# Kernel optimization log

Measured on AMD Instinct MI355X. Metric: run time of the kernel, lower is better.

## Reference

```python
import jax, jax.numpy as jnp
import numpy as np

NUM_HEADS = 2
D = 512
D_HID = 2048


def _layer_norm(x, g, b, eps):
    mu = jnp.mean(x, axis=-1, keepdims=True)
    var = jnp.var(x, axis=-1, keepdims=True)
    return (x - mu) * jax.lax.rsqrt(var + eps) * g + b


def _attn_block(Q, K, V, resnet, Wq, Wk, Wv, ln_g, ln_b, w1, w2, fln_g, fln_b):
    # Linear projections (torch Linear: x @ W.T), no bias
    q = Q @ Wq.T
    k = K @ Wk.T
    v = V @ Wv.T
    B, N, C = q.shape
    gs = C // NUM_HEADS  # group size per head
    # split channels into heads == reshape [B,N,H,gs] -> [B,H,N,gs]
    qh = q.reshape(B, N, NUM_HEADS, gs).transpose(0, 2, 1, 3)
    kh = k.reshape(B, K.shape[1], NUM_HEADS, gs).transpose(0, 2, 1, 3)
    vh = v.reshape(B, V.shape[1], NUM_HEADS, gs).transpose(0, 2, 1, 3)
    scores = jnp.einsum('bhqd,bhkd->bhqk', qh, kh) / jnp.sqrt(jnp.asarray(gs, q.dtype))
    attn = jax.nn.softmax(scores, axis=-1)
    out = jnp.einsum('bhqk,bhkd->bhqd', attn, vh)
    # concat heads back to channel dim
    out = out.transpose(0, 2, 1, 3).reshape(B, N, C)
    x = out + resnet
    x = _layer_norm(x, ln_g, ln_b, 1e-5)
    # FFN (dropout is identity in eval mode)
    residual = x
    y = jax.nn.relu(x @ w1.T) @ w2.T
    y = y + residual
    y = _layer_norm(y, fln_g, fln_b, 1e-6)
    return y


def setup_inputs() -> dict:
    key = jax.random.key(0)
    ks = jax.random.split(key, 16)
    B, N = 4, 2048
    Fm = jax.random.normal(ks[0], (B, N, D), dtype=jnp.float32)
    Fs = jax.random.normal(ks[1], (B, N, D), dtype=jnp.float32)
    Fq = jax.random.normal(ks[2], (B, N, D), dtype=jnp.float32)
    s = 0.02
    Wq = jax.random.normal(ks[3], (3, D, D), dtype=jnp.float32) * s
    Wk = jax.random.normal(ks[4], (3, D, D), dtype=jnp.float32) * s
    Wv = jax.random.normal(ks[5], (3, D, D), dtype=jnp.float32) * s
    ln_g = jnp.ones((3, D), dtype=jnp.float32)
    ln_b = jnp.zeros((3, D), dtype=jnp.float32)
    w1 = jax.random.normal(ks[6], (3, D_HID, D), dtype=jnp.float32) * s
    w2 = jax.random.normal(ks[7], (3, D, D_HID), dtype=jnp.float32) * s
    fln_g = jnp.ones((3, D), dtype=jnp.float32)
    fln_b = jnp.zeros((3, D), dtype=jnp.float32)
    return {"Fm": Fm, "Fs": Fs, "Fq": Fq, "Wq": Wq, "Wk": Wk, "Wv": Wv,
            "ln_g": ln_g, "ln_b": ln_b, "w1": w1, "w2": w2,
            "fln_g": fln_g, "fln_b": fln_b, "out_dim": 512}


def reference(Fm, Fs, Fq, Wq, Wk, Wv, ln_g, ln_b, w1, w2, fln_g, fln_b, out_dim):
    def blk(i, Q, K, V, resnet):
        return _attn_block(Q, K, V, resnet, Wq[i], Wk[i], Wv[i], ln_g[i], ln_b[i],
                           w1[i], w2[i], fln_g[i], fln_b[i])
    css = blk(0, Fs, Fs, Fm, Fm)
    cqq = blk(1, Fq, Fq, Fq, Fq)
    csq = blk(2, cqq, Fs, css, css)
    return csq
```

## Files before the change

kernel.cpp:

```cpp
#include <hip/hip_runtime.h>

typedef __bf16 bf16_t;
typedef __bf16 bf16x8 __attribute__((ext_vector_type(8)));
typedef float  f32x4  __attribute__((ext_vector_type(4)));

#define GAS __attribute__((address_space(1)))
#define LAS __attribute__((address_space(3)))

enum { EPI_BF16 = 0, EPI_RELU = 1 };

__global__ void probe_dtype(const unsigned* __restrict__ lng_bits, int* __restrict__ flag)
{
    *flag = (lng_bits[0] == 0x3F800000u) ? 0 : 1;
}

__global__ __launch_bounds__(256) void conv_any3(
    const void* __restrict__ s0, const void* __restrict__ s1, const void* __restrict__ s2,
    bf16_t* __restrict__ d0, bf16_t* __restrict__ d1, bf16_t* __restrict__ d2,
    const int* __restrict__ flag, int n8)
{
    int i = blockIdx.x * 256 + threadIdx.x;
    if (i >= n8) return;
    const void* src = (blockIdx.z == 0) ? s0 : (blockIdx.z == 1) ? s1 : s2;
    bf16_t*    dst = (blockIdx.z == 0) ? d0 : (blockIdx.z == 1) ? d1 : d2;
    if (*flag == 0) {
        const float4* s = (const float4*)src;
        float4 a = s[i * 2], b = s[i * 2 + 1];
        bf16x8 o = { (bf16_t)a.x, (bf16_t)a.y, (bf16_t)a.z, (bf16_t)a.w,
                     (bf16_t)b.x, (bf16_t)b.y, (bf16_t)b.z, (bf16_t)b.w };
        ((bf16x8*)dst)[i] = o;
    } else {
        ((uint4*)dst)[i] = ((const uint4*)src)[i];
    }
}

__global__ __launch_bounds__(256) void widen_ln4(
    const void* __restrict__ a, const void* __restrict__ b,
    const void* __restrict__ c, const void* __restrict__ d,
    float* __restrict__ dst, const int* __restrict__ flag, int n)
{
    int i = blockIdx.x * 256 + threadIdx.x;
    int seg = i / n, j = i - seg * n;
    if (seg >= 4) return;
    const void* s = (seg == 0) ? a : (seg == 1) ? b : (seg == 2) ? c : d;
    dst[i] = (*flag == 0) ? ((const float*)s)[j]
                          : (float)((const bf16_t*)s)[j];
}

template<int EPI, int TMv, int TNv, bool MULTI>
__global__ __launch_bounds__(256) void gemm_bt(
    const bf16_t* __restrict__ A0, const bf16_t* __restrict__ A1, const bf16_t* __restrict__ A2,
    const bf16_t* __restrict__ B0, const bf16_t* __restrict__ B1, const bf16_t* __restrict__ B2,
    bf16_t* __restrict__ C0, bf16_t* __restrict__ C1, bf16_t* __restrict__ C2,
    int K, int lda, int ldb, int ldc,
    long sAb, long sAh, long sBb, long sBh, long sCb, long sCh,
    float scale)
{
    constexpr int MF = TMv / 32, NF = TNv / 32;
    constexpr int STG = 2 * (TMv + TNv) * 32;
    constexpr int RPK = TMv * TNv;
    constexpr int SME = (STG > RPK) ? STG : RPK;
    __shared__ __align__(16) bf16_t smem[SME];
    bf16_t* Asb = smem;
    bf16_t* Bsb = smem + 2 * TMv * 32;

    const bf16_t* A; const bf16_t* B; bf16_t* C; long cOff = 0;
    if constexpr (MULTI) {
        const int z = blockIdx.z;
        A = (z == 0) ? A0 : (z == 1) ? A1 : A2;
        B = (z == 0) ? B0 : (z == 1) ? B1 : B2;
        C = (z == 0) ? C0 : (z == 1) ? C1 : C2;
    } else {
        const long zb = blockIdx.z >> 1, zh = blockIdx.z & 1;
        A = A0 + zb * sAb + zh * sAh;
        B = B0 + zb * sBb + zh * sBh;
        C = C0; cOff = zb * sCb + zh * sCh;
    }

    int m_t, n_t;
    {
        const int gx = gridDim.x, gy = gridDim.y;
        if ((gy & 7) == 0) {
            const int L = blockIdx.y * gx + blockIdx.x;
            const int band_h = gy >> 3;
            const int r = L >> 3;
            m_t = (L & 7) * band_h + (r % band_h);
            n_t = r / band_h;
        } else { m_t = blockIdx.y; n_t = blockIdx.x; }
    }
    const int n0 = n_t * TNv;
    const int m0 = m_t * TMv;

    const int tid  = threadIdx.x;
    const int wave = tid >> 6, lane = tid & 63;
    const int wm = (wave >> 1) * (TMv / 2);
    const int wn = (wave & 1) * (TNv / 2);
    const int lrow = lane & 15, lquad = lane >> 4;
    const int rq   = (lquad ^ ((lrow >> 1) & 3)) * 8;
    const int drow = lane >> 2;
    const int dcol = (((lane & 3) ^ ((lane >> 3) & 3))) * 8;

    f32x4 acc[MF][NF];
    #pragma unroll
    for (int i = 0; i < MF; i++)
        #pragma unroll
        for (int j = 0; j < NF; j++) acc[i][j] = (f32x4){0.f, 0.f, 0.f, 0.f};

    const bf16_t* aP = A + (long)(m0 + wave * (TMv / 4) + drow) * lda + dcol;
    const bf16_t* bP = B + (long)(n0 + wave * (TNv / 4) + drow) * ldb + dcol;
    bf16_t* asW = Asb + wave * (TMv / 4) * 32;
    bf16_t* bsW = Bsb + wave * (TNv / 4) * 32;

    for (int kk = 0; kk < K; kk += 64) {
        __syncthreads();
        #pragma unroll
        for (int p = 0; p < 2; p++) {
            #pragma unroll
            for (int i = 0; i < TMv / 64; i++)
                __builtin_amdgcn_global_load_lds(
                    (GAS void*)(aP + p * 32 + (long)i * 16 * lda),
                    (LAS void*)(asW + p * TMv * 32 + i * 16 * 32), 16, 0, 0);
            #pragma unroll
            for (int i = 0; i < TNv / 64; i++)
                __builtin_amdgcn_global_load_lds(
                    (GAS void*)(bP + p * 32 + (long)i * 16 * ldb),
                    (LAS void*)(bsW + p * TNv * 32 + i * 16 * 32), 16, 0, 0);
        }
        aP += 64; bP += 64;
        __syncthreads();

        #pragma unroll
        for (int p = 0; p < 2; p++) {
            bf16x8 af[MF], bfr[NF];
            #pragma unroll
            for (int mi = 0; mi < MF; mi++)
                af[mi] = *(const bf16x8*)&Asb[(p * TMv + wm + mi * 16 + lrow) * 32 + rq];
            #pragma unroll
            for (int ni = 0; ni < NF; ni++)
                bfr[ni] = *(const bf16x8*)&Bsb[(p * TNv + wn + ni * 16 + lrow) * 32 + rq];
            #pragma unroll
            for (int mi = 0; mi < MF; mi++)
                #pragma unroll
                for (int ni = 0; ni < NF; ni++)
                    acc[mi][ni] = __builtin_amdgcn_mfma_f32_16x16x32_bf16(
                        af[mi], bfr[ni], acc[mi][ni], 0, 0, 0);
        }
    }

    __syncthreads();
    #pragma unroll
    for (int mi = 0; mi < MF; mi++)
        #pragma unroll
        for (int ni = 0; ni < NF; ni++)
            #pragma unroll
            for (int r = 0; r < 4; r++) {
                float v = acc[mi][ni][r] * scale;
                if (EPI == EPI_RELU) v = fmaxf(v, 0.f);
                smem[(wm + mi * 16 + lquad * 4 + r) * TNv + wn + ni * 16 + lrow] = (bf16_t)v;
            }
    __syncthreads();
    constexpr int TPR = TNv / 8;
    constexpr int RPP = 256 / TPR;
    const int srow = tid / TPR;
    const int scol = (tid % TPR) * 8;
    #pragma unroll
    for (int pass = 0; pass < TMv / RPP; pass++) {
        const int rr = pass * RPP + srow;
        bf16x8 vv = *(const bf16x8*)&smem[rr * TNv + scol];
        *(bf16x8*)&C[cOff + (long)(m0 + rr) * ldc + n0 + scol] = vv;
    }
}

__global__ __launch_bounds__(256) void transpose_v(
    const bf16_t* __restrict__ v, bf16_t* __restrict__ vT)
{
    __shared__ bf16_t t[64][72];
    const int m0 = blockIdx.x * 64;
    const int c0 = blockIdx.y * 64;
    const int tid = threadIdx.x;
    const int rr = tid >> 3;
    const int cc = (tid & 7) * 8;
    #pragma unroll
    for (int i = 0; i < 2; i++) {
        int r = rr + i * 32;
        *(uint4*)&t[r][cc] = *(const uint4*)&v[(long)(m0 + r) * 512 + c0 + cc];
    }
    __syncthreads();
    const int b = m0 >> 11;
    #pragma unroll
    for (int i = 0; i < 2; i++) {
        int d  = rr + i * 32;
        int gc = c0 + d;
        int h  = gc >> 8, dd = gc & 255;
        int n  = (m0 & 2047) + cc;
        bf16x8 tmp;
        #pragma unroll
        for (int j = 0; j < 8; j++) tmp[j] = t[cc + j][d];
        *(bf16x8*)&vT[((long)(b * 2 + h) * 256 + dd) * 2048 + n] = tmp;
    }
}

__global__ __launch_bounds__(256) void softmax_rows(bf16_t* __restrict__ buf)
{
    const long base = (long)blockIdx.x * 2048;
    const int tid = threadIdx.x;
    const int wave = tid >> 6, lane = tid & 63;
    __shared__ float red[8];
    bf16x8 x = *(const bf16x8*)&buf[base + tid * 8];
    float v[8];
    float mx = -1e30f;
    #pragma unroll
    for (int j = 0; j < 8; j++) { v[j] = (float)x[j]; mx = fmaxf(mx, v[j]); }
    for (int off = 32; off; off >>= 1) mx = fmaxf(mx, __shfl_xor(mx, off));
    if (lane == 0) red[wave] = mx;
    __syncthreads();
    mx = fmaxf(fmaxf(red[0], red[1]), fmaxf(red[2], red[3]));
    float s = 0.f;
    #pragma unroll
    for (int j = 0; j < 8; j++) { v[j] = __expf(v[j] - mx); s += v[j]; }
    for (int off = 32; off; off >>= 1) s += __shfl_xor(s, off);
    if (lane == 0) red[4 + wave] = s;
    __syncthreads();
    s = red[4] + red[5] + red[6] + red[7];
    const float inv = 1.f / s;
    bf16x8 y;
    #pragma unroll
    for (int j = 0; j < 8; j++) y[j] = (bf16_t)(v[j] * inv);
    *(bf16x8*)&buf[base + tid * 8] = y;
}

template<typename OutT>
__global__ __launch_bounds__(256) void add_ln(
    const bf16_t* xin, const bf16_t* __restrict__ res,
    const float* __restrict__ g, const float* __restrict__ bias,
    OutT* out, float eps)
{
    const int wave = threadIdx.x >> 6, lane = threadIdx.x & 63;
    const long row = (long)blockIdx.x * 4 + wave;
    const long base = row * 512 + lane * 8;
    bf16x8 a8 = *(const bf16x8*)&xin[base];
    bf16x8 r8 = *(const bf16x8*)&res[base];
    float v[8];
    #pragma unroll
    for (int j = 0; j < 8; j++) v[j] = (float)a8[j] + (float)r8[j];
    float s = 0.f, s2 = 0.f;
    #pragma unroll
    for (int j = 0; j < 8; j++) { s += v[j]; s2 += v[j] * v[j]; }
    for (int off = 32; off; off >>= 1) { s += __shfl_xor(s, off); s2 += __shfl_xor(s2, off); }
    const float mu  = s * (1.f / 512.f);
    const float var = s2 * (1.f / 512.f) - mu * mu;
    const float rs  = rsqrtf(var + eps);
    const int c0 = lane * 8;
    float4 g0 = *(const float4*)&g[c0];
    float4 g1 = *(const float4*)&g[c0 + 4];
    float4 b0 = *(const float4*)&bias[c0];
    float4 b1 = *(const float4*)&bias[c0 + 4];
    float gv[8] = { g0.x, g0.y, g0.z, g0.w, g1.x, g1.y, g1.z, g1.w };
    float bv[8] = { b0.x, b0.y, b0.z, b0.w, b1.x, b1.y, b1.z, b1.w };
    #pragma unroll
    for (int j = 0; j < 8; j++)
        out[base + j] = (OutT)((v[j] - mu) * rs * gv[j] + bv[j]);
}

extern "C" void kernel_launch(void* const* d_in, const int* in_sizes, int n_in,
                              void* d_out, int out_size, void* d_ws, size_t ws_size,
                              hipStream_t stream)
{
    const void* Fm    = d_in[0];
    const void* Fs    = d_in[1];
    const void* Fq    = d_in[2];
    const void* Wq    = d_in[3];
    const void* Wk    = d_in[4];
    const void* Wv    = d_in[5];
    const void* ln_g  = d_in[6];
    const void* ln_b  = d_in[7];
    const void* w1    = d_in[8];
    const void* w2    = d_in[9];
    const void* fln_g = d_in[10];
    const void* fln_b = d_in[11];
    (void)in_sizes; (void)n_in; (void)out_size; (void)ws_size;

    char* ws = (char*)d_ws;
    size_t off = 0;
    auto take = [&](size_t bytes) {
        char* p = ws + off;
        off += (bytes + 255) & ~(size_t)255;
        return p;
    };
    const size_t NT = 8192ul * 512;

    int*    flag = (int*)take(256);
    float*  lnw  = (float*)take(4ul * 1536 * 4);
    bf16_t* Fm_b = (bf16_t*)take(NT * 2);
    bf16_t* Fs_b = (bf16_t*)take(NT * 2);
    bf16_t* Fq_b = (bf16_t*)take(NT * 2);
    bf16_t* wqb  = (bf16_t*)take(3ul * 512 * 512 * 2);
    bf16_t* wkb  = (bf16_t*)take(3ul * 512 * 512 * 2);
    bf16_t* wvb  = (bf16_t*)take(3ul * 512 * 512 * 2);
    bf16_t* w1b  = (bf16_t*)take(3ul * 2048 * 512 * 2);
    bf16_t* w2b  = (bf16_t*)take(3ul * 512 * 2048 * 2);
    bf16_t* q_b  = (bf16_t*)take(NT * 2);
    bf16_t* k_b  = (bf16_t*)take(NT * 2);
    char*   R_v  = take(NT * 2);
    char*   R_vt = take(NT * 2);
    char*   R_sc = take(8ul * 2048 * 2048 * 2);

    bf16_t* css = Fm_b;
    bf16_t* cqq = Fq_b;

    bf16_t* v_b = (bf16_t*)R_v;
    bf16_t* ao  = (bf16_t*)R_v;
    bf16_t* x_b = (bf16_t*)R_v;
    bf16_t* vT  = (bf16_t*)R_vt;
    bf16_t* y_b = (bf16_t*)R_vt;
    bf16_t* sc  = (bf16_t*)R_sc;
    bf16_t* h_b = (bf16_t*)R_sc;

    dim3 blk(256);
    probe_dtype<<<dim3(1), dim3(1), 0, stream>>>((const unsigned*)ln_g, flag);

    conv_any3<<<dim3(2048, 1, 3), blk, 0, stream>>>(
        Fm, Fs, Fq, Fm_b, Fs_b, Fq_b, flag, (int)(NT / 8));
    conv_any3<<<dim3(384, 1, 3), blk, 0, stream>>>(
        Wq, Wk, Wv, wqb, wkb, wvb, flag, (int)(3ul * 512 * 512 / 8));
    conv_any3<<<dim3(1536, 1, 2), blk, 0, stream>>>(
        w1, w2, w2, w1b, w2b, w2b, flag, (int)(3ul * 2048 * 512 / 8));
    widen_ln4<<<dim3(24), blk, 0, stream>>>(ln_g, ln_b, fln_g, fln_b, lnw, flag, 1536);

    auto block = [&](const bf16_t* Q, const bf16_t* Kin, const bf16_t* V,
                     const bf16_t* res, int i, void* outp, bool out_f32) {
        const bf16_t* wqr = wqb + (size_t)i * 512 * 512;
        const bf16_t* wkr = wkb + (size_t)i * 512 * 512;
        const bf16_t* wvr = wvb + (size_t)i * 512 * 512;
        const bf16_t* w1r = w1b + (size_t)i * 2048 * 512;
        const bf16_t* w2r = w2b + (size_t)i * 512 * 2048;
        const float* g1 = lnw + i * 512;
        const float* b1 = lnw + 1536 + i * 512;
        const float* g2 = lnw + 2 * 1536 + i * 512;
        const float* b2 = lnw + 3 * 1536 + i * 512;

        gemm_bt<EPI_BF16, 128, 64, true><<<dim3(8, 64, 3), blk, 0, stream>>>(
            Q, Kin, V, wqr, wkr, wvr, q_b, k_b, v_b,
            512, 512, 512, 512, 0, 0, 0, 0, 0, 0, 1.f);
        transpose_v<<<dim3(128, 8, 1), blk, 0, stream>>>(v_b, vT);

        gemm_bt<EPI_BF16, 128, 128, false><<<dim3(16, 16, 8), blk, 0, stream>>>(
            q_b, nullptr, nullptr, k_b, nullptr, nullptr, sc, nullptr, nullptr,
            256, 512, 512, 2048,
            1048576L, 256L, 1048576L, 256L, 8388608L, 4194304L, 0.0625f);
        softmax_rows<<<dim3(16384), blk, 0, stream>>>(sc);
        gemm_bt<EPI_BF16, 128, 64, false><<<dim3(4, 16, 8), blk, 0, stream>>>(
            sc, nullptr, nullptr, vT, nullptr, nullptr, ao, nullptr, nullptr,
            2048, 2048, 2048, 512,
            8388608L, 4194304L, 1048576L, 524288L, 1048576L, 256L, 1.f);
        add_ln<bf16_t><<<dim3(2048), blk, 0, stream>>>(ao, res, g1, b1, x_b, 1e-5f);

        gemm_bt<EPI_RELU, 128, 128, false><<<dim3(16, 64, 1), blk, 0, stream>>>(
            x_b, nullptr, nullptr, w1r, nullptr, nullptr, h_b, nullptr, nullptr,
            512, 512, 512, 2048, 0, 0, 0, 0, 0, 0, 1.f);
        gemm_bt<EPI_BF16, 128, 64, false><<<dim3(8, 64, 1), blk, 0, stream>>>(
            h_b, nullptr, nullptr, w2r, nullptr, nullptr, y_b, nullptr, nullptr,
            2048, 2048, 2048, 512, 0, 0, 0, 0, 0, 0, 1.f);
        if (out_f32)
            add_ln<float><<<dim3(2048), blk, 0, stream>>>(
                y_b, x_b, g2, b2, (float*)outp, 1e-6f);
        else
            add_ln<bf16_t><<<dim3(2048), blk, 0, stream>>>(
                y_b, x_b, g2, b2, (bf16_t*)outp, 1e-6f);
    };

    block(Fs_b, Fs_b, Fm_b, Fm_b, 0, css, false);
    block(Fq_b, Fq_b, Fq_b, Fq_b, 1, cqq, false);
    block(cqq,  Fs_b, css,  css,  2, d_out, true);
}
```

Before: 697.8 us.

## Batch independent attention blocks 0 and 1 together and fuse V transpose into projection

```diff
diff --git a/kernel.cpp b/kernel.cpp
--- a/kernel.cpp
+++ b/kernel.cpp
@@ -2,12 +2,19 @@
 
 typedef __bf16 bf16_t;
 typedef __bf16 bf16x8 __attribute__((ext_vector_type(8)));
+typedef __bf16 bf16x4 __attribute__((ext_vector_type(4)));
 typedef float  f32x4  __attribute__((ext_vector_type(4)));
 
 #define GAS __attribute__((address_space(1)))
 #define LAS __attribute__((address_space(3)))
 
 enum { EPI_BF16 = 0, EPI_RELU = 1 };
+
+struct GPtrs {
+    const bf16_t* A[6];
+    const bf16_t* B[6];
+    bf16_t*       C[6];
+};
 
 __global__ void probe_dtype(const unsigned* __restrict__ lng_bits, int* __restrict__ flag)
 {
@@ -47,12 +54,9 @@
                           : (float)((const bf16_t*)s)[j];
 }
 
-template<int EPI, int TMv, int TNv, bool MULTI>
+template<int EPI, int TMv, int TNv, bool TABLE, int ZH, bool VT>
 __global__ __launch_bounds__(256) void gemm_bt(
-    const bf16_t* __restrict__ A0, const bf16_t* __restrict__ A1, const bf16_t* __restrict__ A2,
-    const bf16_t* __restrict__ B0, const bf16_t* __restrict__ B1, const bf16_t* __restrict__ B2,
-    bf16_t* __restrict__ C0, bf16_t* __restrict__ C1, bf16_t* __restrict__ C2,
-    int K, int lda, int ldb, int ldc,
+    GPtrs P, int K, int lda, int ldb, int ldc,
     long sAb, long sAh, long sBb, long sBh, long sCb, long sCh,
     float scale)
 {
@@ -64,17 +68,16 @@
     bf16_t* Asb = smem;
     bf16_t* Bsb = smem + 2 * TMv * 32;
 
+    const int z = blockIdx.z;
     const bf16_t* A; const bf16_t* B; bf16_t* C; long cOff = 0;
-    if constexpr (MULTI) {
-        const int z = blockIdx.z;
-        A = (z == 0) ? A0 : (z == 1) ? A1 : A2;
-        B = (z == 0) ? B0 : (z == 1) ? B1 : B2;
-        C = (z == 0) ? C0 : (z == 1) ? C1 : C2;
+    if constexpr (TABLE) {
+        A = P.A[z]; B = P.B[z]; C = P.C[z];
     } else {
-        const long zb = blockIdx.z >> 1, zh = blockIdx.z & 1;
-        A = A0 + zb * sAb + zh * sAh;
-        B = B0 + zb * sBb + zh * sBh;
-        C = C0; cOff = zb * sCb + zh * sCh;
+        const int half = z / ZH, zz = z % ZH;
+        const long zb = zz >> 1, zh = zz & 1;
+        A = P.A[half] + zb * sAb + zh * sAh;
+        B = P.B[half] + zb * sBb + zh * sBh;
+        C = P.C[half]; cOff = zb * sCb + zh * sCh;
     }
 
     int m_t, n_t;
@@ -145,6 +148,24 @@
                     acc[mi][ni] = __builtin_amdgcn_mfma_f32_16x16x32_bf16(
                         af[mi], bfr[ni], acc[mi][ni], 0, 0, 0);
         }
+    }
+
+    if (VT && (z % 3 == 2)) {
+        #pragma unroll
+        for (int mi = 0; mi < MF; mi++)
+            #pragma unroll
+            for (int ni = 0; ni < NF; ni++) {
+                const int mr = m0 + wm + mi * 16 + lquad * 4;
+                const int nc = n0 + wn + ni * 16 + lrow;
+                const int b = mr >> 11, s = mr & 2047;
+                const int h = nc >> 8,  d = nc & 255;
+                bf16x4 t = { (bf16_t)(acc[mi][ni][0]),
+                             (bf16_t)(acc[mi][ni][1]),
+                             (bf16_t)(acc[mi][ni][2]),
+                             (bf16_t)(acc[mi][ni][3]) };
+                *(bf16x4*)&C[(((long)(b * 2 + h) * 256 + d) << 11) + s] = t;
+            }
+        return;
     }
 
     __syncthreads();
@@ -171,35 +192,6 @@
     }
 }
 
-__global__ __launch_bounds__(256) void transpose_v(
-    const bf16_t* __restrict__ v, bf16_t* __restrict__ vT)
-{
-    __shared__ bf16_t t[64][72];
-    const int m0 = blockIdx.x * 64;
-    const int c0 = blockIdx.y * 64;
-    const int tid = threadIdx.x;
-    const int rr = tid >> 3;
-    const int cc = (tid & 7) * 8;
-    #pragma unroll
-    for (int i = 0; i < 2; i++) {
-        int r = rr + i * 32;
-        *(uint4*)&t[r][cc] = *(const uint4*)&v[(long)(m0 + r) * 512 + c0 + cc];
-    }
-    __syncthreads();
-    const int b = m0 >> 11;
-    #pragma unroll
-    for (int i = 0; i < 2; i++) {
-        int d  = rr + i * 32;
-        int gc = c0 + d;
-        int h  = gc >> 8, dd = gc & 255;
-        int n  = (m0 & 2047) + cc;
-        bf16x8 tmp;
-        #pragma unroll
-        for (int j = 0; j < 8; j++) tmp[j] = t[cc + j][d];
-        *(bf16x8*)&vT[((long)(b * 2 + h) * 256 + dd) * 2048 + n] = tmp;
-    }
-}
-
 __global__ __launch_bounds__(256) void softmax_rows(bf16_t* __restrict__ buf)
 {
     const long base = (long)blockIdx.x * 2048;
@@ -229,14 +221,20 @@
     *(bf16x8*)&buf[base + tid * 8] = y;
 }
 
-template<typename OutT>
-__global__ __launch_bounds__(256) void add_ln(
-    const bf16_t* xin, const bf16_t* __restrict__ res,
-    const float* __restrict__ g, const float* __restrict__ bias,
-    OutT* out, float eps)
+__global__ __launch_bounds__(256) void add_ln2(
+    const bf16_t* xA, const bf16_t* rA, const float* gA, const float* bA, bf16_t* oA,
+    const bf16_t* xB, const bf16_t* rB, const float* gB, const float* bB, bf16_t* oB,
+    float eps, int splitRows)
 {
     const int wave = threadIdx.x >> 6, lane = threadIdx.x & 63;
-    const long row = (long)blockIdx.x * 4 + wave;
+    long row = (long)blockIdx.x * 4 + wave;
+    const bf16_t* xin; const bf16_t* res; const float* g; const float* bias; bf16_t* out;
+    if (row >= splitRows) {
+        row -= splitRows;
+        xin = xB; res = rB; g = gB; bias = bB; out = oB;
+    } else {
+        xin = xA; res = rA; g = gA; bias = bA; out = oA;
+    }
     const long base = row * 512 + lane * 8;
     bf16x8 a8 = *(const bf16x8*)&xin[base];
     bf16x8 r8 = *(const bf16x8*)&res[base];
@@ -259,7 +257,39 @@
     float bv[8] = { b0.x, b0.y, b0.z, b0.w, b1.x, b1.y, b1.z, b1.w };
     #pragma unroll
     for (int j = 0; j < 8; j++)
-        out[base + j] = (OutT)((v[j] - mu) * rs * gv[j] + bv[j]);
+        out[base + j] = (bf16_t)((v[j] - mu) * rs * gv[j] + bv[j]);
+}
+
+__global__ __launch_bounds__(256) void add_ln_f32(
+    const bf16_t* xin, const bf16_t* __restrict__ res,
+    const float* __restrict__ g, const float* __restrict__ bias,
+    float* out, float eps)
+{
+    const int wave = threadIdx.x >> 6, lane = threadIdx.x & 63;
+    const long row = (long)blockIdx.x * 4 + wave;
+    const long base = row * 512 + lane * 8;
+    bf16x8 a8 = *(const bf16x8*)&xin[base];
+    bf16x8 r8 = *(const bf16x8*)&res[base];
+    float v[8];
+    #pragma unroll
+    for (int j = 0; j < 8; j++) v[j] = (float)a8[j] + (float)r8[j];
+    float s = 0.f, s2 = 0.f;
+    #pragma unroll
+    for (int j = 0; j < 8; j++) { s += v[j]; s2 += v[j] * v[j]; }
+    for (int off = 32; off; off >>= 1) { s += __shfl_xor(s, off); s2 += __shfl_xor(s2, off); }
+    const float mu  = s * (1.f / 512.f);
+    const float var = s2 * (1.f / 512.f) - mu * mu;
+    const float rs  = rsqrtf(var + eps);
+    const int c0 = lane * 8;
+    float4 g0 = *(const float4*)&g[c0];
+    float4 g1 = *(const float4*)&g[c0 + 4];
+    float4 b0 = *(const float4*)&bias[c0];
+    float4 b1 = *(const float4*)&bias[c0 + 4];
+    float gv[8] = { g0.x, g0.y, g0.z, g0.w, g1.x, g1.y, g1.z, g1.w };
+    float bv[8] = { b0.x, b0.y, b0.z, b0.w, b1.x, b1.y, b1.z, b1.w };
+    #pragma unroll
+    for (int j = 0; j < 8; j++)
+        out[base + j] = (v[j] - mu) * rs * gv[j] + bv[j];
 }
 
 extern "C" void kernel_launch(void* const* d_in, const int* in_sizes, int n_in,
@@ -299,22 +329,25 @@
     bf16_t* wvb  = (bf16_t*)take(3ul * 512 * 512 * 2);
     bf16_t* w1b  = (bf16_t*)take(3ul * 2048 * 512 * 2);
     bf16_t* w2b  = (bf16_t*)take(3ul * 512 * 2048 * 2);
-    bf16_t* q_b  = (bf16_t*)take(NT * 2);
-    bf16_t* k_b  = (bf16_t*)take(NT * 2);
-    char*   R_v  = take(NT * 2);
-    char*   R_vt = take(NT * 2);
-    char*   R_sc = take(8ul * 2048 * 2048 * 2);
-
+    bf16_t* q0   = (bf16_t*)take(NT * 2);
+    bf16_t* k0   = (bf16_t*)take(NT * 2);
+    bf16_t* q1   = (bf16_t*)take(NT * 2);
+    bf16_t* k1   = (bf16_t*)take(NT * 2);
+    bf16_t* vT0  = (bf16_t*)take(NT * 2);
+    bf16_t* vT1  = (bf16_t*)take(NT * 2);
+    bf16_t* scb  = (bf16_t*)take(2ul * 8 * 2048 * 2048 * 2);
+
+    bf16_t* sc0 = scb;
+    bf16_t* sc1 = scb + 8ul * 2048 * 2048;
+    bf16_t* ao0 = q0;  bf16_t* ao1 = q1;
+    bf16_t* x0  = k0;  bf16_t* x1  = k1;
+    bf16_t* h0  = scb; bf16_t* h1  = scb + 16ul * 1024 * 1024;
+    bf16_t* y0  = vT0; bf16_t* y1  = vT1;
     bf16_t* css = Fm_b;
     bf16_t* cqq = Fq_b;
-
-    bf16_t* v_b = (bf16_t*)R_v;
-    bf16_t* ao  = (bf16_t*)R_v;
-    bf16_t* x_b = (bf16_t*)R_v;
-    bf16_t* vT  = (bf16_t*)R_vt;
-    bf16_t* y_b = (bf16_t*)R_vt;
-    bf16_t* sc  = (bf16_t*)R_sc;
-    bf16_t* h_b = (bf16_t*)R_sc;
+    bf16_t* q2  = q0;  bf16_t* k2  = k0;  bf16_t* vT2 = vT0;
+    bf16_t* sc2 = scb; bf16_t* ao2 = q1;  bf16_t* x2  = k1;
+    bf16_t* h2  = scb + 32ul * 1024 * 1024;  bf16_t* y2 = vT1;
 
     dim3 blk(256);
     probe_dtype<<<dim3(1), dim3(1), 0, stream>>>((const unsigned*)ln_g, flag);
@@ -327,49 +360,94 @@
         w1, w2, w2, w1b, w2b, w2b, flag, (int)(3ul * 2048 * 512 / 8));
     widen_ln4<<<dim3(24), blk, 0, stream>>>(ln_g, ln_b, fln_g, fln_b, lnw, flag, 1536);
 
-    auto block = [&](const bf16_t* Q, const bf16_t* Kin, const bf16_t* V,
-                     const bf16_t* res, int i, void* outp, bool out_f32) {
-        const bf16_t* wqr = wqb + (size_t)i * 512 * 512;
-        const bf16_t* wkr = wkb + (size_t)i * 512 * 512;
-        const bf16_t* wvr = wvb + (size_t)i * 512 * 512;
-        const bf16_t* w1r = w1b + (size_t)i * 2048 * 512;
-        const bf16_t* w2r = w2b + (size_t)i * 512 * 2048;
-        const float* g1 = lnw + i * 512;
-        const float* b1 = lnw + 1536 + i * 512;
-        const float* g2 = lnw + 2 * 1536 + i * 512;
-        const float* b2 = lnw + 3 * 1536 + i * 512;
-
-        gemm_bt<EPI_BF16, 128, 64, true><<<dim3(8, 64, 3), blk, 0, stream>>>(
-            Q, Kin, V, wqr, wkr, wvr, q_b, k_b, v_b,
-            512, 512, 512, 512, 0, 0, 0, 0, 0, 0, 1.f);
-        transpose_v<<<dim3(128, 8, 1), blk, 0, stream>>>(v_b, vT);
-
-        gemm_bt<EPI_BF16, 128, 128, false><<<dim3(16, 16, 8), blk, 0, stream>>>(
-            q_b, nullptr, nullptr, k_b, nullptr, nullptr, sc, nullptr, nullptr,
-            256, 512, 512, 2048,
+    auto W  = [&](bf16_t* base, int i, size_t n) { return (const bf16_t*)(base + (size_t)i * n); };
+    const float* g1[3]; const float* b1[3]; const float* g2[3]; const float* b2[3];
+    for (int i = 0; i < 3; i++) {
+        g1[i] = lnw + i * 512;            b1[i] = lnw + 1536 + i * 512;
+        g2[i] = lnw + 2 * 1536 + i * 512; b2[i] = lnw + 3 * 1536 + i * 512;
+    }
+
+    {
+        GPtrs P{};
+        P.A[0] = Fs_b; P.A[1] = Fs_b; P.A[2] = Fm_b;
+        P.A[3] = Fq_b; P.A[4] = Fq_b; P.A[5] = Fq_b;
+        P.B[0] = W(wqb, 0, 512*512); P.B[1] = W(wkb, 0, 512*512); P.B[2] = W(wvb, 0, 512*512);
+        P.B[3] = W(wqb, 1, 512*512); P.B[4] = W(wkb, 1, 512*512); P.B[5] = W(wvb, 1, 512*512);
+        P.C[0] = q0; P.C[1] = k0; P.C[2] = vT0;
+        P.C[3] = q1; P.C[4] = k1; P.C[5] = vT1;
+        gemm_bt<EPI_BF16, 128, 64, true, 1, true><<<dim3(8, 64, 6), blk, 0, stream>>>(
+            P, 512, 512, 512, 512, 0, 0, 0, 0, 0, 0, 1.f);
+    }
+    {
+        GPtrs P{}; P.A[0] = q0; P.A[1] = q1; P.B[0] = k0; P.B[1] = k1;
+        P.C[0] = sc0; P.C[1] = sc1;
+        gemm_bt<EPI_BF16, 128, 128, false, 8, false><<<dim3(16, 16, 16), blk, 0, stream>>>(
+            P, 256, 512, 512, 2048,
             1048576L, 256L, 1048576L, 256L, 8388608L, 4194304L, 0.0625f);
-        softmax_rows<<<dim3(16384), blk, 0, stream>>>(sc);
-        gemm_bt<EPI_BF16, 128, 64, false><<<dim3(4, 16, 8), blk, 0, stream>>>(
-            sc, nullptr, nullptr, vT, nullptr, nullptr, ao, nullptr, nullptr,
-            2048, 2048, 2048, 512,
+    }
+    softmax_rows<<<dim3(32768), blk, 0, stream>>>(scb);
+    {
+        GPtrs P{}; P.A[0] = sc0; P.A[1] = sc1; P.B[0] = vT0; P.B[1] = vT1;
+        P.C[0] = ao0; P.C[1] = ao1;
+        gemm_bt<EPI_BF16, 128, 64, false, 8, false><<<dim3(4, 16, 16), blk, 0, stream>>>(
+            P, 2048, 2048, 2048, 512,
             8388608L, 4194304L, 1048576L, 524288L, 1048576L, 256L, 1.f);
-        add_ln<bf16_t><<<dim3(2048), blk, 0, stream>>>(ao, res, g1, b1, x_b, 1e-5f);
-
-        gemm_bt<EPI_RELU, 128, 128, false><<<dim3(16, 64, 1), blk, 0, stream>>>(
-            x_b, nullptr, nullptr, w1r, nullptr, nullptr, h_b, nullptr, nullptr,
-            512, 512, 512, 2048, 0, 0, 0, 0, 0, 0, 1.f);
-        gemm_bt<EPI_BF16, 128, 64, false><<<dim3(8, 64, 1), blk, 0, stream>>>(
-            h_b, nullptr, nullptr, w2r, nullptr, nullptr, y_b, nullptr, nullptr,
-            2048, 2048, 2048, 512, 0, 0, 0, 0, 0, 0, 1.f);
-        if (out_f32)
-            add_ln<float><<<dim3(2048), blk, 0, stream>>>(
-                y_b, x_b, g2, b2, (float*)outp, 1e-6f);
-        else
-            add_ln<bf16_t><<<dim3(2048), blk, 0, stream>>>(
-                y_b, x_b, g2, b2, (bf16_t*)outp, 1e-6f);
-    };
-
-    block(Fs_b, Fs_b, Fm_b, Fm_b, 0, css, false);
-    block(Fq_b, Fq_b, Fq_b, Fq_b, 1, cqq, false);
-    block(cqq,  Fs_b, css,  css,  2, d_out, true);
-}
+    }
+    add_ln2<<<dim3(4096), blk, 0, stream>>>(
+        ao0, Fm_b, g1[0], b1[0], x0,
+        ao1, Fq_b, g1[1], b1[1], x1, 1e-5f, 8192);
+    {
+        GPtrs P{}; P.A[0] = x0; P.A[1] = x1;
+        P.B[0] = W(w1b, 0, 2048*512); P.B[1] = W(w1b, 1, 2048*512);
+        P.C[0] = h0; P.C[1] = h1;
+        gemm_bt<EPI_RELU, 128, 128, false, 1, false><<<dim3(16, 64, 2), blk, 0, stream>>>(
+            P, 512, 512, 512, 2048, 0, 0, 0, 0, 0, 0, 1.f);
+    }
+    {
+        GPtrs P{}; P.A[0] = h0; P.A[1] = h1;
+        P.B[0] = W(w2b, 0, 512*2048); P.B[1] = W(w2b, 1, 512*2048);
+        P.C[0] = y0; P.C[1] = y1;
+        gemm_bt<EPI_BF16, 128, 64, false, 1, false><<<dim3(8, 64, 2), blk, 0, stream>>>(
+            P, 2048, 2048, 2048, 512, 0, 0, 0, 0, 0, 0, 1.f);
+    }
+    add_ln2<<<dim3(4096), blk, 0, stream>>>(
+        y0, x0, g2[0], b2[0], css,
+        y1, x1, g2[1], b2[1], cqq, 1e-6f, 8192);
+
+    {
+        GPtrs P{};
+        P.A[0] = cqq; P.A[1] = Fs_b; P.A[2] = css;
+        P.B[0] = W(wqb, 2, 512*512); P.B[1] = W(wkb, 2, 512*512); P.B[2] = W(wvb, 2, 512*512);
+        P.C[0] = q2; P.C[1] = k2; P.C[2] = vT2;
+        gemm_bt<EPI_BF16, 128, 64, true, 1, true><<<dim3(8, 64, 3), blk, 0, stream>>>(
+            P, 512, 512, 512, 512, 0, 0, 0, 0, 0, 0, 1.f);
+    }
+    {
+        GPtrs P{}; P.A[0] = q2; P.B[0] = k2; P.C[0] = sc2;
+        gemm_bt<EPI_BF16, 128, 128, false, 8, false><<<dim3(16, 16, 8), blk, 0, stream>>>(
+            P, 256, 512, 512, 2048,
+            1048576L, 256L, 1048576L, 256L, 8388608L, 4194304L, 0.0625f);
+    }
+    softmax_rows<<<dim3(16384), blk, 0, stream>>>(sc2);
+    {
+        GPtrs P{}; P.A[0] = sc2; P.B[0] = vT2; P.C[0] = ao2;
+        gemm_bt<EPI_BF16, 128, 64, false, 8, false><<<dim3(4, 16, 8), blk, 0, stream>>>(
+            P, 2048, 2048, 2048, 512,
+            8388608L, 4194304L, 1048576L, 524288L, 1048576L, 256L, 1.f);
+    }
+    add_ln2<<<dim3(2048), blk, 0, stream>>>(
+        ao2, css, g1[2], b1[2], x2,
+        ao2, css, g1[2], b1[2], x2, 1e-5f, 1 << 30);
+    {
+        GPtrs P{}; P.A[0] = x2; P.B[0] = W(w1b, 2, 2048*512); P.C[0] = h2;
+        gemm_bt<EPI_RELU, 128, 128, false, 1, false><<<dim3(16, 64, 1), blk, 0, stream>>>(
+            P, 512, 512, 512, 2048, 0, 0, 0, 0, 0, 0, 1.f);
+    }
+    {
+        GPtrs P{}; P.A[0] = h2; P.B[0] = W(w2b, 2, 512*2048); P.C[0] = y2;
+        gemm_bt<EPI_BF16, 128, 64, false, 1, false><<<dim3(8, 64, 1), blk, 0, stream>>>(
+            P, 2048, 2048, 2048, 512, 0, 0, 0, 0, 0, 0, 1.f);
+    }
+    add_ln_f32<<<dim3(2048), blk, 0, stream>>>(
+        y2, x2, g2[2], b2[2], (float*)d_out, 1e-6f);
+}
```

Result: faster. 624.6 us (-10.5%).
